# Kernel tuning notes

Measured on AMD Instinct MI355X. Metric: run time of the kernel, lower is better.

The kernel has to match this reference:

```python
import jax, jax.numpy as jnp
import numpy as np

T = 16384       # video length (frames)
C = 7           # out_features = d_model = num surgical phases
F_DIM = 2048    # mstcn_f_dim (spatial feature dim)
LEN_Q = 30      # sliding window length
N_HEADS = 4
D_K = 64        # attn_dim = min(64, mstcn_f_maps=64)
D_FF = 64       # d_ff = mstcn_f_maps


def setup_inputs() -> dict:
    key = jax.random.key(0)
    ks = jax.random.split(key, 10)
    w = lambda i, shape: jax.random.normal(ks[i], shape, jnp.float32) * 0.05
    return {
        "x": jax.random.normal(ks[0], (1, C, T), jnp.float32),
        "long_feature": jax.random.normal(ks[1], (1, T, F_DIM), jnp.float32),
        "W_fc": w(2, (C, F_DIM)),              # nn.Linear(mstcn_f_dim, out_features, bias=False)
        "W_q": w(3, (N_HEADS * D_K, C)),
        "W_k": w(4, (N_HEADS * D_K, C)),
        "W_v": w(5, (N_HEADS * D_K, C)),
        "W_o": w(6, (C, N_HEADS * D_K)),
        "ln1_g": jnp.ones((C,), jnp.float32),
        "ln1_b": jnp.zeros((C,), jnp.float32),
        "W_ff1": w(7, (D_FF, C)),
        "W_ff2": w(8, (C, D_FF)),
        "ln2_g": jnp.ones((C,), jnp.float32),
        "ln2_b": jnp.zeros((C,), jnp.float32),
    }


def layer_norm(x, g, b, eps=1e-5):
    mu = x.mean(-1, keepdims=True)
    var = ((x - mu) ** 2).mean(-1, keepdims=True)
    return (x - mu) * jax.lax.rsqrt(var + eps) * g + b


def reference(x, long_feature, W_fc, W_q, W_k, W_v, W_o, ln1_g, ln1_b, W_ff1, W_ff2, ln2_g, ln2_b):
    # --- vectorized sliding-window (replaces the Python loop of zeros/cat/stack) ---
    feats = x[0].T                                            # (T, C)
    padded = jnp.concatenate([jnp.zeros((LEN_Q - 1, C), feats.dtype), feats], axis=0)
    idx = jnp.arange(T)[:, None] + jnp.arange(LEN_Q)[None, :]  # window ends at frame i
    inputs = padded[idx]                                       # (T, LEN_Q, C)

    # --- spatial embedding: feas = tanh(fc(long_feature)).transpose(0,1) ---
    feas = jnp.tanh(long_feature[0] @ W_fc.T)[:, None, :]      # (T, 1, C)

    # --- decoder layer: cross MHA(query=feas, kv=inputs) + residual + LN ---
    q = (feas @ W_q.T).reshape(T, 1, N_HEADS, D_K).transpose(0, 2, 1, 3)       # (T,H,1,Dk)
    k = (inputs @ W_k.T).reshape(T, LEN_Q, N_HEADS, D_K).transpose(0, 2, 1, 3)  # (T,H,Lq,Dk)
    v = (inputs @ W_v.T).reshape(T, LEN_Q, N_HEADS, D_K).transpose(0, 2, 1, 3)  # (T,H,Lq,Dk)
    scores = jnp.einsum('thqd,thkd->thqk', q, k) / np.float32(np.sqrt(D_K))
    attn = jax.nn.softmax(scores, axis=-1)
    ctx = jnp.einsum('thqk,thkd->thqd', attn, v)
    ctx = ctx.transpose(0, 2, 1, 3).reshape(T, 1, N_HEADS * D_K)
    out = layer_norm(ctx @ W_o.T + feas, ln1_g, ln1_b)         # (T, 1, C)

    # --- position-wise FFN + residual + LN ---
    ff = jax.nn.relu(out @ W_ff1.T) @ W_ff2.T
    out = layer_norm(ff + out, ln2_g, ln2_b)
    return out[:, 0]                                           # (T, C) per-frame logits
```

## Files before the change

kernel.cpp:

```cpp
#include <hip/hip_runtime.h>
#include <math.h>

#define T_FRAMES 16384
#define FDIM 2048
#define LQ 30

__global__ __launch_bounds__(448) void setup_kernel(
    const float* __restrict__ Wq, const float* __restrict__ Wk,
    const float* __restrict__ Wv, const float* __restrict__ Wo,
    float* __restrict__ AM) {
  const int e = threadIdx.x;
  if (e >= 392) return;
  const int which = e / 196;
  const int r = e % 196;
  const int h = r / 49;
  const int rr = r % 49;
  const int c = rr / 7;
  const int c2 = rr % 7;
  float s = 0.0f;
  if (which == 0) {
    for (int d = 0; d < 64; ++d)
      s = fmaf(Wq[(h * 64 + d) * 7 + c], Wk[(h * 64 + d) * 7 + c2], s);
  } else {
    for (int d = 0; d < 64; ++d)
      s = fmaf(Wo[c * 256 + h * 64 + d], Wv[(h * 64 + d) * 7 + c2], s);
  }
  AM[e] = s;
}

#define FPB_A 8

__global__ __launch_bounds__(256) void feas_kernel(
    const float* __restrict__ lf,
    const float* __restrict__ Wfc,
    float* __restrict__ feas) {
  const int tid = threadIdx.x;
  const int lane = tid & 63;
  const int wave = tid >> 6;
  const int t0 = blockIdx.x * FPB_A + wave * 2;
  const float* lfp = lf + (size_t)t0 * FDIM + lane * 4;

  float4 a0[8], a1[8];
#pragma unroll
  for (int ch = 0; ch < 8; ++ch) a0[ch] = *(const float4*)(lfp + ch * 256);
#pragma unroll
  for (int ch = 0; ch < 8; ++ch) a1[ch] = *(const float4*)(lfp + FDIM + ch * 256);

  float acc0[7] = {0, 0, 0, 0, 0, 0, 0};
  float acc1[7] = {0, 0, 0, 0, 0, 0, 0};
#pragma unroll
  for (int ch = 0; ch < 8; ++ch) {
#pragma unroll
    for (int c = 0; c < 7; ++c) {
      const float4 w = *(const float4*)(Wfc + c * FDIM + ch * 256 + lane * 4);
      acc0[c] = fmaf(a0[ch].x, w.x, fmaf(a0[ch].y, w.y,
                fmaf(a0[ch].z, w.z, fmaf(a0[ch].w, w.w, acc0[c]))));
      acc1[c] = fmaf(a1[ch].x, w.x, fmaf(a1[ch].y, w.y,
                fmaf(a1[ch].z, w.z, fmaf(a1[ch].w, w.w, acc1[c]))));
    }
  }

#pragma unroll
  for (int c = 0; c < 7; ++c) {
    float v0 = acc0[c];
    float v1 = acc1[c];
#pragma unroll
    for (int off = 32; off > 0; off >>= 1) {
      v0 += __shfl_down(v0, off, 64);
      v1 += __shfl_down(v1, off, 64);
    }
    if (lane == 0) {
      feas[(size_t)t0 * 7 + c]       = tanhf(v0);
      feas[(size_t)(t0 + 1) * 7 + c] = tanhf(v1);
    }
  }
}

#define BF 64

__global__ __launch_bounds__(256) void attn_kernel(
    const float* __restrict__ x,
    const float* __restrict__ feas_g,
    const float* __restrict__ AM,
    const float* __restrict__ W1,
    const float* __restrict__ W2,
    const float* __restrict__ ln1g, const float* __restrict__ ln1b,
    const float* __restrict__ ln2g, const float* __restrict__ ln2b,
    float* __restrict__ out) {
  __shared__ float AM_s[392];
  __shared__ float ft[(BF + LQ - 1) * 7];
  __shared__ float feas_s[BF][7];
  __shared__ float hpart[BF][4][7];

  const int tid = threadIdx.x;
  const int t0 = blockIdx.x * BF;

  for (int i = tid; i < 392; i += 256) AM_s[i] = AM[i];
  for (int i = tid; i < (BF + LQ - 1) * 7; i += 256) {
    const int row = i / 7, c = i % 7;
    const int s = t0 - (LQ - 1) + row;
    ft[i] = (s >= 0) ? x[c * T_FRAMES + s] : 0.0f;
  }
  for (int i = tid; i < BF * 7; i += 256)
    feas_s[i / 7][i % 7] = feas_g[(size_t)t0 * 7 + i];
  __syncthreads();

  {
    const int f = tid >> 2;
    const int h = tid & 3;
    float fe[7];
#pragma unroll
    for (int c = 0; c < 7; ++c) fe[c] = feas_s[f][c];

    const float* Ah = AM_s + h * 49;
    const float* Mh = AM_s + 196 + h * 49;
    float qk[7];
#pragma unroll
    for (int c2 = 0; c2 < 7; ++c2) {
      float s = 0.0f;
#pragma unroll
      for (int c = 0; c < 7; ++c) s = fmaf(fe[c], Ah[c * 7 + c2], s);
      qk[c2] = s * 0.125f;
    }
    const float* frow = &ft[f * 7];
    float sc[LQ];
    float m = -1e30f;
#pragma unroll
    for (int j = 0; j < LQ; ++j) {
      const float* r = frow + j * 7;
      float s = 0.0f;
#pragma unroll
      for (int c2 = 0; c2 < 7; ++c2) s = fmaf(qk[c2], r[c2], s);
      sc[j] = s;
      m = fmaxf(m, s);
    }
    float sum = 0.0f;
    float wsum[7] = {0, 0, 0, 0, 0, 0, 0};
#pragma unroll
    for (int j = 0; j < LQ; ++j) {
      const float p = __expf(sc[j] - m);
      sum += p;
      const float* r = frow + j * 7;
#pragma unroll
      for (int c2 = 0; c2 < 7; ++c2) wsum[c2] = fmaf(p, r[c2], wsum[c2]);
    }
    const float inv = 1.0f / sum;
#pragma unroll
    for (int c = 0; c < 7; ++c) {
      float s = 0.0f;
#pragma unroll
      for (int c2 = 0; c2 < 7; ++c2) s = fmaf(Mh[c * 7 + c2], wsum[c2], s);
      hpart[f][h][c] = s * inv;
    }
  }
  __syncthreads();

  if (tid < BF) {
    const int f = tid;
    float v[7];
#pragma unroll
    for (int c = 0; c < 7; ++c)
      v[c] = feas_s[f][c] + hpart[f][0][c] + hpart[f][1][c] + hpart[f][2][c] + hpart[f][3][c];

    float mu = 0.0f;
#pragma unroll
    for (int c = 0; c < 7; ++c) mu += v[c];
    mu *= (1.0f / 7.0f);
    float var = 0.0f;
#pragma unroll
    for (int c = 0; c < 7; ++c) { const float d = v[c] - mu; var = fmaf(d, d, var); }
    var *= (1.0f / 7.0f);
    float rs = rsqrtf(var + 1e-5f);
    float o1[7];
#pragma unroll
    for (int c = 0; c < 7; ++c) o1[c] = (v[c] - mu) * rs * ln1g[c] + ln1b[c];

    float ff[7] = {0, 0, 0, 0, 0, 0, 0};
    for (int k = 0; k < 64; ++k) {
      float hk = 0.0f;
#pragma unroll
      for (int c = 0; c < 7; ++c) hk = fmaf(W1[k * 7 + c], o1[c], hk);
      hk = fmaxf(hk, 0.0f);
#pragma unroll
      for (int c = 0; c < 7; ++c) ff[c] = fmaf(W2[c * 64 + k], hk, ff[c]);
    }

#pragma unroll
    for (int c = 0; c < 7; ++c) v[c] = ff[c] + o1[c];
    mu = 0.0f;
#pragma unroll
    for (int c = 0; c < 7; ++c) mu += v[c];
    mu *= (1.0f / 7.0f);
    var = 0.0f;
#pragma unroll
    for (int c = 0; c < 7; ++c) { const float d = v[c] - mu; var = fmaf(d, d, var); }
    var *= (1.0f / 7.0f);
    rs = rsqrtf(var + 1e-5f);
    const int t = t0 + f;
#pragma unroll
    for (int c = 0; c < 7; ++c)
      out[(size_t)t * 7 + c] = (v[c] - mu) * rs * ln2g[c] + ln2b[c];
  }
}

extern "C" void kernel_launch(void* const* d_in, const int* in_sizes, int n_in,
                              void* d_out, int out_size, void* d_ws, size_t ws_size,
                              hipStream_t stream) {
  const float* x    = (const float*)d_in[0];
  const float* lf   = (const float*)d_in[1];
  const float* Wfc  = (const float*)d_in[2];
  const float* Wq   = (const float*)d_in[3];
  const float* Wk   = (const float*)d_in[4];
  const float* Wv   = (const float*)d_in[5];
  const float* Wo   = (const float*)d_in[6];
  const float* ln1g = (const float*)d_in[7];
  const float* ln1b = (const float*)d_in[8];
  const float* W1   = (const float*)d_in[9];
  const float* W2   = (const float*)d_in[10];
  const float* ln2g = (const float*)d_in[11];
  const float* ln2b = (const float*)d_in[12];
  float* out = (float*)d_out;

  float* AM = (float*)d_ws;

  setup_kernel<<<1, 448, 0, stream>>>(Wq, Wk, Wv, Wo, AM);
  feas_kernel<<<T_FRAMES / FPB_A, 256, 0, stream>>>(lf, Wfc, out);
  attn_kernel<<<T_FRAMES / BF, 256, 0, stream>>>(
      x, out, AM, W1, W2, ln1g, ln1b, ln2g, ln2b, out);
}
```

Baseline: 277.3 us.

## Stage swizzled transposed W_fc in shared memory for feature projection

Adds a pre-kernel that transposes W_fc into a channel-interleaved, XOR-swizzled layout in workspace. The feature projection kernel then loads it once per block into 64 KB of shared memory and processes 32 frames per block, with 16 lanes per frame. This replaces repeated global weight loads per frame with LDS reads and uses narrower 16-lane reductions. The large shared memory footprint lowers occupancy, and an extra small launch is added.

```diff
diff --git a/kernel.cpp b/kernel.cpp
--- a/kernel.cpp
+++ b/kernel.cpp
@@ -4,6 +4,8 @@
 #define T_FRAMES 16384
 #define FDIM 2048
 #define LQ 30
+#define FB 32
+#define BF 64
 
 __global__ __launch_bounds__(448) void setup_kernel(
     const float* __restrict__ Wq, const float* __restrict__ Wk,
@@ -28,55 +30,76 @@
   AM[e] = s;
 }
 
-#define FPB_A 8
+__global__ __launch_bounds__(1024) void wfct_kernel(
+    const float* __restrict__ Wfc, float* __restrict__ WT) {
+  const int i = blockIdx.x * 1024 + threadIdx.x;
+  if (i >= 512 * 32) return;
+  const int k4 = i >> 5, slot = i & 31;
+  const int key = k4 & 7;
+  const int c = (slot >> 2) ^ key;
+  const int e = slot & 3;
+  WT[i] = (c < 7) ? Wfc[c * FDIM + k4 * 4 + e] : 0.0f;
+}
 
 __global__ __launch_bounds__(256) void feas_kernel(
     const float* __restrict__ lf,
-    const float* __restrict__ Wfc,
+    const float* __restrict__ WT,
     float* __restrict__ feas) {
-  const int tid = threadIdx.x;
+  __shared__ float wt[512 * 32];
+  __shared__ float red[8][4][7];
+
+  const int tid  = threadIdx.x;
   const int lane = tid & 63;
   const int wave = tid >> 6;
-  const int t0 = blockIdx.x * FPB_A + wave * 2;
-  const float* lfp = lf + (size_t)t0 * FDIM + lane * 4;
-
-  float4 a0[8], a1[8];
-#pragma unroll
-  for (int ch = 0; ch < 8; ++ch) a0[ch] = *(const float4*)(lfp + ch * 256);
-#pragma unroll
-  for (int ch = 0; ch < 8; ++ch) a1[ch] = *(const float4*)(lfp + FDIM + ch * 256);
-
-  float acc0[7] = {0, 0, 0, 0, 0, 0, 0};
-  float acc1[7] = {0, 0, 0, 0, 0, 0, 0};
-#pragma unroll
-  for (int ch = 0; ch < 8; ++ch) {
+  const int t0   = blockIdx.x * FB;
+
+  {
+    const float4* s = (const float4*)WT;
+    float4* d = (float4*)wt;
+#pragma unroll
+    for (int i = 0; i < 16; ++i) d[tid + i * 256] = s[tid + i * 256];
+  }
+  __syncthreads();
+
+  const int fs  = lane >> 4;
+  const int l16 = lane & 15;
+  const int key = l16 & 7;
+
+  for (int qi = 0; qi < 2; ++qi) {
+    const int q = wave + qi * 4;
+    const float* rowp = lf + (size_t)(t0 + q * 4 + fs) * FDIM;
+
+    float acc[7] = {0, 0, 0, 0, 0, 0, 0};
+#pragma unroll 4
+    for (int j = 0; j < 32; ++j) {
+      const float4 a = *(const float4*)(rowp + j * 64 + l16 * 4);
+      const float* wbase = wt + (j * 16 + l16) * 32;
+#pragma unroll
+      for (int c = 0; c < 7; ++c) {
+        const float4 w = *(const float4*)(wbase + ((c ^ key) << 2));
+        acc[c] = fmaf(a.x, w.x, fmaf(a.y, w.y,
+                 fmaf(a.z, w.z, fmaf(a.w, w.w, acc[c]))));
+      }
+    }
+
 #pragma unroll
     for (int c = 0; c < 7; ++c) {
-      const float4 w = *(const float4*)(Wfc + c * FDIM + ch * 256 + lane * 4);
-      acc0[c] = fmaf(a0[ch].x, w.x, fmaf(a0[ch].y, w.y,
-                fmaf(a0[ch].z, w.z, fmaf(a0[ch].w, w.w, acc0[c]))));
-      acc1[c] = fmaf(a1[ch].x, w.x, fmaf(a1[ch].y, w.y,
-                fmaf(a1[ch].z, w.z, fmaf(a1[ch].w, w.w, acc1[c]))));
-    }
-  }
-
-#pragma unroll
-  for (int c = 0; c < 7; ++c) {
-    float v0 = acc0[c];
-    float v1 = acc1[c];
-#pragma unroll
-    for (int off = 32; off > 0; off >>= 1) {
-      v0 += __shfl_down(v0, off, 64);
-      v1 += __shfl_down(v1, off, 64);
-    }
-    if (lane == 0) {
-      feas[(size_t)t0 * 7 + c]       = tanhf(v0);
-      feas[(size_t)(t0 + 1) * 7 + c] = tanhf(v1);
-    }
-  }
-}
-
-#define BF 64
+      acc[c] += __shfl_xor(acc[c], 1, 16);
+      acc[c] += __shfl_xor(acc[c], 2, 16);
+      acc[c] += __shfl_xor(acc[c], 4, 16);
+      acc[c] += __shfl_xor(acc[c], 8, 16);
+    }
+    float v = acc[0];
+#pragma unroll
+    for (int c = 1; c < 7; ++c)
+      if (l16 == c) v = acc[c];
+    if (l16 < 7) red[q][fs][l16] = v;
+  }
+  __syncthreads();
+
+  if (tid < FB * 7)
+    feas[(size_t)t0 * 7 + tid] = tanhf(((const float*)red)[tid]);
+}
 
 __global__ __launch_bounds__(256) void attn_kernel(
     const float* __restrict__ x,
@@ -222,9 +245,11 @@
   float* out = (float*)d_out;
 
   float* AM = (float*)d_ws;
+  float* WT = (float*)d_ws + 512;
 
   setup_kernel<<<1, 448, 0, stream>>>(Wq, Wk, Wv, Wo, AM);
-  feas_kernel<<<T_FRAMES / FPB_A, 256, 0, stream>>>(lf, Wfc, out);
+  wfct_kernel<<<16, 1024, 0, stream>>>(Wfc, WT);
+  feas_kernel<<<T_FRAMES / FB, 256, 0, stream>>>(lf, WT, out);
   attn_kernel<<<T_FRAMES / BF, 256, 0, stream>>>(
       x, out, AM, W1, W2, ln1g, ln1b, ln2g, ln2b, out);
 }
```

Measured after the change: 245.0 us. 11.7% less time.

## Stream long_feature with nontemporal loads and use DPP wave reductions in feas kernel

Applied to the files above, without the earlier changes.

The feas kernel now loads long_feature rows chunk by chunk with nontemporal loads inside a partially unrolled loop, instead of preloading all 16 float4 values per lane. This lowers register pressure, and a launch-bounds occupancy hint is added. The shuffle-down reduction is replaced by DPP row operations plus two xor shuffles, and the tanh and store work is spread across 14 lanes instead of being done serially by lane 0. The kernel is bound by streaming 128MB of input, so the gains depend on whether higher occupancy and the cache hint improve bandwidth, while less load-level parallelism per wave is the risk.

```diff
diff --git a/kernel.cpp b/kernel.cpp
--- a/kernel.cpp
+++ b/kernel.cpp
@@ -4,6 +4,9 @@
 #define T_FRAMES 16384
 #define FDIM 2048
 #define LQ 30
+#define BF 64
+
+typedef float f4 __attribute__((ext_vector_type(4)));
 
 __global__ __launch_bounds__(448) void setup_kernel(
     const float* __restrict__ Wq, const float* __restrict__ Wk,
@@ -28,55 +31,61 @@
   AM[e] = s;
 }
 
-#define FPB_A 8
-
-__global__ __launch_bounds__(256) void feas_kernel(
+template <int CTRL>
+__device__ __forceinline__ float dpp_add(float v) {
+  const int s =
+      __builtin_amdgcn_update_dpp(0, __float_as_int(v), CTRL, 0xF, 0xF, true);
+  return v + __int_as_float(s);
+}
+
+__global__ __launch_bounds__(256, 6) void feas_kernel(
     const float* __restrict__ lf,
     const float* __restrict__ Wfc,
     float* __restrict__ feas) {
-  const int tid = threadIdx.x;
+  const int tid  = threadIdx.x;
   const int lane = tid & 63;
   const int wave = tid >> 6;
-  const int t0 = blockIdx.x * FPB_A + wave * 2;
-  const float* lfp = lf + (size_t)t0 * FDIM + lane * 4;
-
-  float4 a0[8], a1[8];
-#pragma unroll
-  for (int ch = 0; ch < 8; ++ch) a0[ch] = *(const float4*)(lfp + ch * 256);
-#pragma unroll
-  for (int ch = 0; ch < 8; ++ch) a1[ch] = *(const float4*)(lfp + FDIM + ch * 256);
+  const int t0   = (blockIdx.x * 4 + wave) * 2;
+  const float* rowp = lf + (size_t)t0 * FDIM + lane * 4;
 
   float acc0[7] = {0, 0, 0, 0, 0, 0, 0};
   float acc1[7] = {0, 0, 0, 0, 0, 0, 0};
-#pragma unroll
+
+#pragma unroll 2
   for (int ch = 0; ch < 8; ++ch) {
+    const f4 a0 = __builtin_nontemporal_load((const f4*)(rowp + ch * 256));
+    const f4 a1 = __builtin_nontemporal_load((const f4*)(rowp + FDIM + ch * 256));
 #pragma unroll
     for (int c = 0; c < 7; ++c) {
-      const float4 w = *(const float4*)(Wfc + c * FDIM + ch * 256 + lane * 4);
-      acc0[c] = fmaf(a0[ch].x, w.x, fmaf(a0[ch].y, w.y,
-                fmaf(a0[ch].z, w.z, fmaf(a0[ch].w, w.w, acc0[c]))));
-      acc1[c] = fmaf(a1[ch].x, w.x, fmaf(a1[ch].y, w.y,
-                fmaf(a1[ch].z, w.z, fmaf(a1[ch].w, w.w, acc1[c]))));
+      const f4 w = *(const f4*)(Wfc + c * FDIM + ch * 256 + lane * 4);
+      acc0[c] = fmaf(a0.x, w.x, fmaf(a0.y, w.y,
+                fmaf(a0.z, w.z, fmaf(a0.w, w.w, acc0[c]))));
+      acc1[c] = fmaf(a1.x, w.x, fmaf(a1.y, w.y,
+                fmaf(a1.z, w.z, fmaf(a1.w, w.w, acc1[c]))));
     }
   }
 
 #pragma unroll
   for (int c = 0; c < 7; ++c) {
-    float v0 = acc0[c];
-    float v1 = acc1[c];
-#pragma unroll
-    for (int off = 32; off > 0; off >>= 1) {
-      v0 += __shfl_down(v0, off, 64);
-      v1 += __shfl_down(v1, off, 64);
-    }
-    if (lane == 0) {
-      feas[(size_t)t0 * 7 + c]       = tanhf(v0);
-      feas[(size_t)(t0 + 1) * 7 + c] = tanhf(v1);
-    }
-  }
-}
-
-#define BF 64
+    float v0 = acc0[c], v1 = acc1[c];
+    v0 = dpp_add<0xB1>(v0);   v1 = dpp_add<0xB1>(v1);
+    v0 = dpp_add<0x4E>(v0);   v1 = dpp_add<0x4E>(v1);
+    v0 = dpp_add<0x141>(v0);  v1 = dpp_add<0x141>(v1);
+    v0 = dpp_add<0x140>(v0);  v1 = dpp_add<0x140>(v1);
+    v0 += __shfl_xor(v0, 16, 64);  v1 += __shfl_xor(v1, 16, 64);
+    v0 += __shfl_xor(v0, 32, 64);  v1 += __shfl_xor(v1, 32, 64);
+    acc0[c] = v0;  acc1[c] = v1;
+  }
+
+  float v = acc0[0];
+#pragma unroll
+  for (int c = 1; c < 7; ++c)
+    if (lane == c) v = acc0[c];
+#pragma unroll
+  for (int c = 0; c < 7; ++c)
+    if (lane == 7 + c) v = acc1[c];
+  if (lane < 14) feas[(size_t)t0 * 7 + lane] = tanhf(v);
+}
 
 __global__ __launch_bounds__(256) void attn_kernel(
     const float* __restrict__ x,
@@ -224,7 +233,7 @@
   float* AM = (float*)d_ws;
 
   setup_kernel<<<1, 448, 0, stream>>>(Wq, Wk, Wv, Wo, AM);
-  feas_kernel<<<T_FRAMES / FPB_A, 256, 0, stream>>>(lf, Wfc, out);
+  feas_kernel<<<T_FRAMES / 8, 256, 0, stream>>>(lf, Wfc, out);
   attn_kernel<<<T_FRAMES / BF, 256, 0, stream>>>(
       x, out, AM, W1, W2, ln1g, ln1b, ln2g, ln2b, out);
 }
```

Result: faster. 243.1 us (-12.3%).
